# Performance work log

Measured on AMD Instinct MI355X. Metric: run time of the kernel, lower is better.

Reference implementation:

```python
import jax, jax.numpy as jnp
import numpy as np

N = 100000
SAMPLE = 25
FEAT = 128
HIDDEN = 128
CLASSES = 40


def setup_inputs() -> dict:
    key = jax.random.key(0)
    k_x, k_n, k_w1, k_w2, k_wl = jax.random.split(key, 5)
    X = jax.random.normal(k_x, (N, FEAT), dtype=jnp.float32)
    neighbors = jax.random.randint(k_n, (N, SAMPLE), 0, N, dtype=jnp.int32)
    # torch Linear weights are [out_features, in_features], xavier-uniform init
    def xavier(k, out_d, in_d):
        bound = float(np.sqrt(6.0 / (in_d + out_d)))
        return jax.random.uniform(k, (out_d, in_d), dtype=jnp.float32, minval=-bound, maxval=bound)
    W1 = xavier(k_w1, HIDDEN, FEAT)
    W2 = xavier(k_w2, HIDDEN, HIDDEN)
    Wlast = xavier(k_wl, CLASSES, HIDDEN)
    return {"X": X, "neighbors": neighbors, "W1": W1, "W2": W2, "Wlast": Wlast}


def reference(X, neighbors, W1, W2, Wlast):
    # forward: for each layer W: X = spmm(adj, X); X = X @ W.T; relu(X)
    # adj row i has sample_num entries of value 1/sample_num -> mean over sampled neighbors
    h = X
    for W in (W1, W2):
        agg = jnp.mean(h[neighbors], axis=1)          # [N, sample, d] -> [N, d]
        h = jax.nn.relu(jnp.einsum('nd,hd->nh', agg, W))
    return jnp.einsum('nh,ch->nc', h, Wlast)          # [N, class_num]
```

## Files before the change

kernel.cpp:

```cpp
#include <hip/hip_runtime.h>
#include <cstdint>
#include <cstddef>

typedef unsigned short u16;
typedef __bf16 bf16x8 __attribute__((ext_vector_type(8)));
typedef u16 u16x8 __attribute__((ext_vector_type(8)));
typedef float f32x4 __attribute__((ext_vector_type(4)));

#define N_NODES 100000
#define SAMPLE 25
#define FEAT 128
#define CLASSES 40

__device__ __forceinline__ float bf2f(u16 v) {
    return __uint_as_float(((unsigned)v) << 16);
}
__device__ __forceinline__ u16 f2bf(float f) {
    unsigned u = __float_as_uint(f);
    u += 0x7FFFu + ((u >> 16) & 1u);
    return (u16)(u >> 16);
}
__device__ __forceinline__ void split_bf(float x, u16& hi, u16& lo) {
    hi = f2bf(x);
    lo = f2bf(x - bf2f(hi));
}

__device__ __forceinline__ void split8(const float* ap, bf16x8& ah, bf16x8& al) {
    union { u16x8 u; bf16x8 b; } H, L;
    #pragma unroll
    for (int j = 0; j < 8; ++j) {
        u16 h, lo; split_bf(ap[j], h, lo);
        H.u[j] = h; L.u[j] = lo;
    }
    ah = H.b; al = L.b;
}

__device__ __forceinline__ f32x4 mfma_split(bf16x8 ah, bf16x8 al,
                                            bf16x8 bh, bf16x8 bl, f32x4 acc) {
    acc = __builtin_amdgcn_mfma_f32_16x16x32_bf16(ah, bh, acc, 0, 0, 0);
    acc = __builtin_amdgcn_mfma_f32_16x16x32_bf16(al, bh, acc, 0, 0, 0);
    acc = __builtin_amdgcn_mfma_f32_16x16x32_bf16(ah, bl, acc, 0, 0, 0);
    return acc;
}

__global__ __launch_bounds__(256) void prep_all(
    const float* __restrict__ X,
    const float* __restrict__ W1, const float* __restrict__ W2,
    const float* __restrict__ Wl,
    u16* __restrict__ xb,
    u16* __restrict__ w1h, u16* __restrict__ w1l,
    u16* __restrict__ w2h, u16* __restrict__ w2l,
    u16* __restrict__ wlh, u16* __restrict__ wll)
{
    const int i = blockIdx.x * 256 + threadIdx.x;
    const int stride = gridDim.x * 256;

    const int nv = (N_NODES * FEAT) / 8;
    for (int v = i; v < nv; v += stride) {
        f32x4 a = *(const f32x4*)(X + (size_t)v * 8);
        f32x4 b = *(const f32x4*)(X + (size_t)v * 8 + 4);
        u16x8 o;
        o[0] = f2bf(a[0]); o[1] = f2bf(a[1]); o[2] = f2bf(a[2]); o[3] = f2bf(a[3]);
        o[4] = f2bf(b[0]); o[5] = f2bf(b[1]); o[6] = f2bf(b[2]); o[7] = f2bf(b[3]);
        *(u16x8*)(xb + (size_t)v * 8) = o;
    }
    for (int j = i; j < FEAT * FEAT; j += stride) {
        split_bf(W1[j], w1h[j], w1l[j]);
        split_bf(W2[j], w2h[j], w2l[j]);
    }
    for (int j = i; j < CLASSES * FEAT; j += stride) {
        split_bf(Wl[j], wlh[j], wll[j]);
    }
}

#define NPB32 32
#define ZT_STRIDE 136

__global__ __launch_bounds__(128, 2) void hopA(
    const u16* __restrict__ Xb, const int* __restrict__ nb,
    const u16* __restrict__ w1h, const u16* __restrict__ w1l,
    const u16* __restrict__ w2h, const u16* __restrict__ w2l,
    u16* __restrict__ Z2)
{
    __shared__ int nbs[NPB32 * SAMPLE];
    __shared__ u16 agg_h[NPB32][ZT_STRIDE];
    __shared__ u16 agg_l[NPB32][ZT_STRIDE];

    const int t = threadIdx.x;
    const int blockStart = blockIdx.x * NPB32;

    for (int i = t; i < NPB32 * SAMPLE; i += 128)
        nbs[i] = nb[blockStart * SAMPLE + i];
    __syncthreads();

    #pragma unroll 1
    for (int it = 0; it < 4; ++it) {
        const int item = t + it * 128;
        const int nl = item >> 4;
        const int fg = item & 15;
        const int* myn = &nbs[nl * SAMPLE];
        u16x8 buf[SAMPLE];
        #pragma unroll
        for (int s = 0; s < SAMPLE; ++s)
            buf[s] = *(const u16x8*)(Xb + ((size_t)myn[s] << 7) + fg * 8);
        float acc[8];
        #pragma unroll
        for (int j = 0; j < 8; ++j) acc[j] = 0.f;
        #pragma unroll
        for (int s = 0; s < SAMPLE; ++s) {
            #pragma unroll
            for (int j = 0; j < 8; ++j) acc[j] += bf2f(buf[s][j]);
        }
        u16x8 oh, ol;
        #pragma unroll
        for (int j = 0; j < 8; ++j) {
            const float m = acc[j] * (1.0f / SAMPLE);
            u16 h, lo; split_bf(m, h, lo);
            oh[j] = h; ol[j] = lo;
        }
        *(u16x8*)&agg_h[nl][fg * 8] = oh;
        *(u16x8*)&agg_l[nl][fg * 8] = ol;
    }
    __syncthreads();

    const int w  = t >> 6;
    const int l  = t & 63;
    const int lr = l & 15;
    const int lq = l >> 4;

    f32x4 hacc[8];
    {
        bf16x8 ah[4], al[4];
        #pragma unroll
        for (int k = 0; k < 4; ++k) {
            ah[k] = *(const bf16x8*)&agg_h[w * 16 + lr][k * 32 + lq * 8];
            al[k] = *(const bf16x8*)&agg_l[w * 16 + lr][k * 32 + lq * 8];
        }
        #pragma unroll
        for (int c = 0; c < 8; ++c) {
            f32x4 acc = {0.f, 0.f, 0.f, 0.f};
            #pragma unroll
            for (int k = 0; k < 4; ++k) {
                const size_t off = (size_t)(c * 16 + lr) * FEAT + k * 32 + lq * 8;
                bf16x8 bh = *(const bf16x8*)(w1h + off);
                bf16x8 bl = *(const bf16x8*)(w1l + off);
                acc = mfma_split(ah[k], al[k], bh, bl, acc);
            }
            hacc[c] = acc;
        }
    }
    __syncthreads();

    #pragma unroll
    for (int c = 0; c < 8; ++c) {
        #pragma unroll
        for (int r = 0; r < 4; ++r) {
            float v = hacc[c][r] > 0.f ? hacc[c][r] : 0.f;
            u16 h, l2; split_bf(v, h, l2);
            agg_h[w * 16 + lq * 4 + r][c * 16 + lr] = h;
            agg_l[w * 16 + lq * 4 + r][c * 16 + lr] = l2;
        }
    }
    __syncthreads();

    {
        bf16x8 ah[4], al[4];
        #pragma unroll
        for (int k = 0; k < 4; ++k) {
            ah[k] = *(const bf16x8*)&agg_h[w * 16 + lr][k * 32 + lq * 8];
            al[k] = *(const bf16x8*)&agg_l[w * 16 + lr][k * 32 + lq * 8];
        }
        __syncthreads();

        #pragma unroll
        for (int c = 0; c < 8; ++c) {
            f32x4 acc = {0.f, 0.f, 0.f, 0.f};
            #pragma unroll
            for (int k = 0; k < 4; ++k) {
                const size_t off = (size_t)(c * 16 + lr) * FEAT + k * 32 + lq * 8;
                bf16x8 bh = *(const bf16x8*)(w2h + off);
                bf16x8 bl = *(const bf16x8*)(w2l + off);
                acc = mfma_split(ah[k], al[k], bh, bl, acc);
            }
            #pragma unroll
            for (int r = 0; r < 4; ++r)
                agg_h[w * 16 + lq * 4 + r][c * 16 + lr] = f2bf(acc[r]);
        }
    }
    __syncthreads();

    #pragma unroll
    for (int p = 0; p < 4; ++p) {
        const int idx = p * 128 + t;
        const int row = idx >> 4;
        const int col = (idx & 15) * 8;
        *(u16x8*)(Z2 + (size_t)(blockStart + row) * FEAT + col) =
            *(const u16x8*)&agg_h[row][col];
    }
}

__global__ __launch_bounds__(128, 3) void hopB(
    const u16* __restrict__ Zin, const int* __restrict__ nb,
    const u16* __restrict__ wh, const u16* __restrict__ wl,
    float* __restrict__ out)
{
    __shared__ int nbs[NPB32 * SAMPLE];
    __shared__ float agg[NPB32][132];

    const int t = threadIdx.x;
    const int blockStart = blockIdx.x * NPB32;

    for (int i = t; i < NPB32 * SAMPLE; i += 128)
        nbs[i] = nb[blockStart * SAMPLE + i];
    __syncthreads();

    #pragma unroll 1
    for (int it = 0; it < 4; ++it) {
        const int item = t + it * 128;
        const int nl = item >> 4;
        const int fg = item & 15;
        const int* myn = &nbs[nl * SAMPLE];
        u16x8 buf[SAMPLE];
        #pragma unroll
        for (int s = 0; s < SAMPLE; ++s)
            buf[s] = *(const u16x8*)(Zin + ((size_t)myn[s] << 7) + fg * 8);
        float acc[8];
        #pragma unroll
        for (int j = 0; j < 8; ++j) acc[j] = 0.f;
        #pragma unroll
        for (int s = 0; s < SAMPLE; ++s) {
            #pragma unroll
            for (int j = 0; j < 8; ++j) acc[j] += bf2f(buf[s][j]);
        }
        #pragma unroll
        for (int j = 0; j < 8; ++j) {
            float m = acc[j] * (1.0f / SAMPLE);
            agg[nl][fg * 8 + j] = m > 0.f ? m : 0.f;
        }
    }
    __syncthreads();

    const int w  = t >> 6;
    const int l  = t & 63;
    const int lr = l & 15;
    const int lq = l >> 4;

    bf16x8 ah[4], al[4];
    #pragma unroll
    for (int k = 0; k < 4; ++k)
        split8(&agg[w * 16 + lr][k * 32 + lq * 8], ah[k], al[k]);

    #pragma unroll
    for (int c = 0; c < 3; ++c) {
        const int o = c * 16 + lr;
        f32x4 acc = {0.f, 0.f, 0.f, 0.f};
        #pragma unroll
        for (int k = 0; k < 4; ++k) {
            bf16x8 bh, bl;
            if (o < CLASSES) {
                const size_t off = (size_t)o * FEAT + k * 32 + lq * 8;
                bh = *(const bf16x8*)(wh + off);
                bl = *(const bf16x8*)(wl + off);
            } else {
                #pragma unroll
                for (int j = 0; j < 8; ++j) { bh[j] = (__bf16)0.f; bl[j] = (__bf16)0.f; }
            }
            acc = mfma_split(ah[k], al[k], bh, bl, acc);
        }
        if (o < CLASSES) {
            #pragma unroll
            for (int r = 0; r < 4; ++r) {
                const int node = blockStart + w * 16 + lq * 4 + r;
                out[(size_t)node * CLASSES + o] = acc[r];
            }
        }
    }
}

#define NPB 64
#define AGG_STRIDE 136

__global__ __launch_bounds__(256) void gnn_layer1(
    const float* __restrict__ X, const int* __restrict__ nb,
    const u16* __restrict__ w1h, const u16* __restrict__ w1l,
    u16* __restrict__ h1)
{
    __shared__ int nbs[NPB * SAMPLE];
    __shared__ u16 agg_h[NPB][AGG_STRIDE];
    __shared__ u16 agg_l[NPB][AGG_STRIDE];

    const int t = threadIdx.x;
    const int blockStart = blockIdx.x * NPB;

    for (int i = t; i < NPB * SAMPLE; i += 256) {
        int gi = blockStart * SAMPLE + i;
        if (gi >= N_NODES * SAMPLE) gi = N_NODES * SAMPLE - 1;
        nbs[i] = nb[gi];
    }
    __syncthreads();

    for (int item = t; item < NPB * 16; item += 256) {
        const int nl = item >> 4;
        const int fg = item & 15;
        float acc[8];
        #pragma unroll
        for (int j = 0; j < 8; ++j) acc[j] = 0.f;
        const int* myn = &nbs[nl * SAMPLE];
        for (int s = 0; s < SAMPLE; ++s) {
            const float4* p = (const float4*)(X + (size_t)myn[s] * FEAT + fg * 8);
            float4 a = p[0], b = p[1];
            acc[0] += a.x; acc[1] += a.y; acc[2] += a.z; acc[3] += a.w;
            acc[4] += b.x; acc[5] += b.y; acc[6] += b.z; acc[7] += b.w;
        }
        u16x8 oh, ol;
        #pragma unroll
        for (int j = 0; j < 8; ++j) {
            float m = acc[j] * (1.0f / SAMPLE);
            u16 h, lo; split_bf(m, h, lo);
            oh[j] = h; ol[j] = lo;
        }
        *(u16x8*)&agg_h[nl][fg * 8] = oh;
        *(u16x8*)&agg_l[nl][fg * 8] = ol;
    }
    __syncthreads();

    const int w  = t >> 6;
    const int l  = t & 63;
    const int lr = l & 15;
    const int lq = l >> 4;

    bf16x8 ah[4], al[4];
    #pragma unroll
    for (int k = 0; k < 4; ++k) {
        ah[k] = *(const bf16x8*)&agg_h[w * 16 + lr][k * 32 + lq * 8];
        al[k] = *(const bf16x8*)&agg_l[w * 16 + lr][k * 32 + lq * 8];
    }

    #pragma unroll
    for (int c = 0; c < 8; ++c) {
        f32x4 acc = {0.f, 0.f, 0.f, 0.f};
        #pragma unroll
        for (int k = 0; k < 4; ++k) {
            const size_t off = (size_t)(c * 16 + lr) * FEAT + k * 32 + lq * 8;
            bf16x8 bh = *(const bf16x8*)(w1h + off);
            bf16x8 bl = *(const bf16x8*)(w1l + off);
            acc = mfma_split(ah[k], al[k], bh, bl, acc);
        }
        #pragma unroll
        for (int r = 0; r < 4; ++r) {
            int node = blockStart + w * 16 + lq * 4 + r;
            if (node < N_NODES) {
                float v = acc[r] > 0.f ? acc[r] : 0.f;
                h1[(size_t)node * FEAT + c * 16 + lr] = f2bf(v);
            }
        }
    }
}

__global__ __launch_bounds__(256) void gnn_layer2_final(
    const u16* __restrict__ h1, const int* __restrict__ nb,
    const u16* __restrict__ w2h, const u16* __restrict__ w2l,
    const u16* __restrict__ wlh, const u16* __restrict__ wll,
    float* __restrict__ out)
{
    __shared__ int nbs[NPB * SAMPLE];
    __shared__ u16 agg_h[NPB][AGG_STRIDE];
    __shared__ u16 agg_l[NPB][AGG_STRIDE];

    const int t = threadIdx.x;
    const int blockStart = blockIdx.x * NPB;

    for (int i = t; i < NPB * SAMPLE; i += 256) {
        int gi = blockStart * SAMPLE + i;
        if (gi >= N_NODES * SAMPLE) gi = N_NODES * SAMPLE - 1;
        nbs[i] = nb[gi];
    }
    __syncthreads();

    for (int item = t; item < NPB * 16; item += 256) {
        const int nl = item >> 4;
        const int fg = item & 15;
        float acc[8];
        #pragma unroll
        for (int j = 0; j < 8; ++j) acc[j] = 0.f;
        const int* myn = &nbs[nl * SAMPLE];
        for (int s = 0; s < SAMPLE; ++s) {
            u16x8 v = *(const u16x8*)(h1 + (size_t)myn[s] * FEAT + fg * 8);
            #pragma unroll
            for (int j = 0; j < 8; ++j) acc[j] += bf2f(v[j]);
        }
        u16x8 oh, ol;
        #pragma unroll
        for (int j = 0; j < 8; ++j) {
            float m = acc[j] * (1.0f / SAMPLE);
            u16 h, lo; split_bf(m, h, lo);
            oh[j] = h; ol[j] = lo;
        }
        *(u16x8*)&agg_h[nl][fg * 8] = oh;
        *(u16x8*)&agg_l[nl][fg * 8] = ol;
    }
    __syncthreads();

    const int w  = t >> 6;
    const int l  = t & 63;
    const int lr = l & 15;
    const int lq = l >> 4;

    f32x4 hacc[8];
    {
        bf16x8 ah[4], al[4];
        #pragma unroll
        for (int k = 0; k < 4; ++k) {
            ah[k] = *(const bf16x8*)&agg_h[w * 16 + lr][k * 32 + lq * 8];
            al[k] = *(const bf16x8*)&agg_l[w * 16 + lr][k * 32 + lq * 8];
        }
        #pragma unroll
        for (int c = 0; c < 8; ++c) {
            f32x4 acc = {0.f, 0.f, 0.f, 0.f};
            #pragma unroll
            for (int k = 0; k < 4; ++k) {
                const size_t off = (size_t)(c * 16 + lr) * FEAT + k * 32 + lq * 8;
                bf16x8 bh = *(const bf16x8*)(w2h + off);
                bf16x8 bl = *(const bf16x8*)(w2l + off);
                acc = mfma_split(ah[k], al[k], bh, bl, acc);
            }
            hacc[c] = acc;
        }
    }
    __syncthreads();

    #pragma unroll
    for (int c = 0; c < 8; ++c) {
        #pragma unroll
        for (int r = 0; r < 4; ++r) {
            float v = hacc[c][r] > 0.f ? hacc[c][r] : 0.f;
            u16 h, l2; split_bf(v, h, l2);
            agg_h[w * 16 + lq * 4 + r][c * 16 + lr] = h;
            agg_l[w * 16 + lq * 4 + r][c * 16 + lr] = l2;
        }
    }
    __syncthreads();

    {
        bf16x8 ah[4], al[4];
        #pragma unroll
        for (int k = 0; k < 4; ++k) {
            ah[k] = *(const bf16x8*)&agg_h[w * 16 + lr][k * 32 + lq * 8];
            al[k] = *(const bf16x8*)&agg_l[w * 16 + lr][k * 32 + lq * 8];
        }
        #pragma unroll
        for (int c = 0; c < 3; ++c) {
            const int o = c * 16 + lr;
            f32x4 acc = {0.f, 0.f, 0.f, 0.f};
            #pragma unroll
            for (int k = 0; k < 4; ++k) {
                bf16x8 bh, bl;
                if (o < CLASSES) {
                    const size_t off = (size_t)o * FEAT + k * 32 + lq * 8;
                    bh = *(const bf16x8*)(wlh + off);
                    bl = *(const bf16x8*)(wll + off);
                } else {
                    #pragma unroll
                    for (int j = 0; j < 8; ++j) { bh[j] = (__bf16)0.f; bl[j] = (__bf16)0.f; }
                }
                acc = mfma_split(ah[k], al[k], bh, bl, acc);
            }
            if (o < CLASSES) {
                #pragma unroll
                for (int r = 0; r < 4; ++r) {
                    int node = blockStart + w * 16 + lq * 4 + r;
                    if (node < N_NODES) {
                        out[(size_t)node * CLASSES + o] = acc[r];
                    }
                }
            }
        }
    }
}

extern "C" void kernel_launch(void* const* d_in, const int* in_sizes, int n_in,
                              void* d_out, int out_size, void* d_ws, size_t ws_size,
                              hipStream_t stream) {
    const float* X  = (const float*)d_in[0];
    const int*   nb = (const int*)d_in[1];
    const float* W1 = (const float*)d_in[2];
    const float* W2 = (const float*)d_in[3];
    const float* Wl = (const float*)d_in[4];
    float* out = (float*)d_out;

    const size_t zelems = (size_t)N_NODES * FEAT;
    const size_t welems = 4 * (size_t)FEAT * FEAT + 2 * (size_t)CLASSES * FEAT;
    const size_t need_fast = (2 * zelems + welems) * sizeof(u16);

    if (ws_size >= need_fast) {
        u16* Xb  = (u16*)d_ws;
        u16* Z2  = Xb + zelems;
        u16* w1h = Z2 + zelems;
        u16* w1l = w1h + FEAT * FEAT;
        u16* w2h = w1l + FEAT * FEAT;
        u16* w2l = w2h + FEAT * FEAT;
        u16* wlh = w2l + FEAT * FEAT;
        u16* wll = wlh + CLASSES * FEAT;

        prep_all<<<512, 256, 0, stream>>>(X, W1, W2, Wl, Xb,
                                          w1h, w1l, w2h, w2l, wlh, wll);
        const int blocks = N_NODES / NPB32;
        hopA<<<blocks, 128, 0, stream>>>(Xb, nb, w1h, w1l, w2h, w2l, Z2);
        hopB<<<blocks, 128, 0, stream>>>(Z2, nb, wlh, wll, out);
    } else {
        u16* h1  = (u16*)d_ws;
        u16* w1h = h1 + zelems;
        u16* w1l = w1h + FEAT * FEAT;
        u16* w2h = w1l + FEAT * FEAT;
        u16* w2l = w2h + FEAT * FEAT;
        u16* wlh = w2l + FEAT * FEAT;
        u16* wll = wlh + CLASSES * FEAT;

        prep_all<<<512, 256, 0, stream>>>(X, W1, W2, Wl,
                                           h1,
                                          w1h, w1l, w2h, w2l, wlh, wll);
        const int blocks = (N_NODES + NPB - 1) / NPB;
        gnn_layer1<<<blocks, 256, 0, stream>>>(X, nb, w1h, w1l, h1);
        gnn_layer2_final<<<blocks, 256, 0, stream>>>(h1, nb, w2h, w2l, wlh, wll, out);
    }
}
```

Measured before the change: 341.3 us.

## Fuse prep and both hops into one persistent cooperative kernel

Replaces the three separate launches (prep, hopA, hopB) with a single cooperative persistent kernel. It uses grid.sync between phases and an atomic work counter so each block pulls 32-node groups dynamically. The aim is to remove launch gaps and tail effects between kernels and to balance load across CUs. In exchange it needs cooperative launch support, adds grid-wide barrier cost, and depends on an occupancy query, falling back to the old path if that query or the launch fails.

```diff
diff --git a/kernel.cpp b/kernel.cpp
--- a/kernel.cpp
+++ b/kernel.cpp
@@ -1,6 +1,9 @@
 #include <hip/hip_runtime.h>
+#include <hip/hip_cooperative_groups.h>
 #include <cstdint>
 #include <cstddef>
+
+namespace cg = cooperative_groups;
 
 typedef unsigned short u16;
 typedef __bf16 bf16x8 __attribute__((ext_vector_type(8)));
@@ -41,6 +44,244 @@
     acc = __builtin_amdgcn_mfma_f32_16x16x32_bf16(al, bh, acc, 0, 0, 0);
     acc = __builtin_amdgcn_mfma_f32_16x16x32_bf16(ah, bl, acc, 0, 0, 0);
     return acc;
+}
+
+#define NPB32 32
+#define ZT_STRIDE 136
+#define NGROUPS 3125
+
+__global__ __launch_bounds__(128, 3) void fused_all(
+    const float* __restrict__ X, const int* __restrict__ nb,
+    const float* __restrict__ W1, const float* __restrict__ W2,
+    const float* __restrict__ Wl,
+    u16* __restrict__ Xb, u16* __restrict__ Z2,
+    u16* __restrict__ w1h, u16* __restrict__ w1l,
+    u16* __restrict__ w2h, u16* __restrict__ w2l,
+    u16* __restrict__ wlh, u16* __restrict__ wll,
+    int* __restrict__ ctr,
+    float* __restrict__ out)
+{
+    __shared__ int nbs[NPB32 * SAMPLE];
+    __shared__ __align__(16) char smembig[2 * NPB32 * ZT_STRIDE * 2];
+    u16 (*agg_h)[ZT_STRIDE] = (u16(*)[ZT_STRIDE])smembig;
+    u16 (*agg_l)[ZT_STRIDE] = (u16(*)[ZT_STRIDE])(smembig + NPB32 * ZT_STRIDE * 2);
+    float (*aggf)[132] = (float(*)[132])smembig;
+    __shared__ int g_sh;
+
+    const int t = threadIdx.x;
+    cg::grid_group grid = cg::this_grid();
+
+    {
+        if (blockIdx.x == 0 && t == 0) { ctr[0] = 0; ctr[1] = 0; }
+        const int i = blockIdx.x * 128 + t;
+        const int stride = gridDim.x * 128;
+        const int nv = (N_NODES * FEAT) / 8;
+        for (int v = i; v < nv; v += stride) {
+            f32x4 a = *(const f32x4*)(X + (size_t)v * 8);
+            f32x4 b = *(const f32x4*)(X + (size_t)v * 8 + 4);
+            u16x8 o;
+            o[0] = f2bf(a[0]); o[1] = f2bf(a[1]); o[2] = f2bf(a[2]); o[3] = f2bf(a[3]);
+            o[4] = f2bf(b[0]); o[5] = f2bf(b[1]); o[6] = f2bf(b[2]); o[7] = f2bf(b[3]);
+            *(u16x8*)(Xb + (size_t)v * 8) = o;
+        }
+        for (int j = i; j < FEAT * FEAT; j += stride) {
+            split_bf(W1[j], w1h[j], w1l[j]);
+            split_bf(W2[j], w2h[j], w2l[j]);
+        }
+        for (int j = i; j < CLASSES * FEAT; j += stride) {
+            split_bf(Wl[j], wlh[j], wll[j]);
+        }
+    }
+    grid.sync();
+
+    const int w  = t >> 6;
+    const int l  = t & 63;
+    const int lr = l & 15;
+    const int lq = l >> 4;
+
+    for (;;) {
+        __syncthreads();
+        if (t == 0) g_sh = atomicAdd(&ctr[0], 1);
+        __syncthreads();
+        const int gid = g_sh;
+        if (gid >= NGROUPS) break;
+        const int blockStart = gid * NPB32;
+
+        for (int i = t; i < NPB32 * SAMPLE; i += 128)
+            nbs[i] = nb[blockStart * SAMPLE + i];
+        __syncthreads();
+
+        #pragma unroll 1
+        for (int it = 0; it < 4; ++it) {
+            const int item = t + it * 128;
+            const int nl = item >> 4;
+            const int fg = item & 15;
+            const int* myn = &nbs[nl * SAMPLE];
+            u16x8 buf[SAMPLE];
+            #pragma unroll
+            for (int s = 0; s < SAMPLE; ++s)
+                buf[s] = *(const u16x8*)(Xb + ((size_t)myn[s] << 7) + fg * 8);
+            float acc[8];
+            #pragma unroll
+            for (int j = 0; j < 8; ++j) acc[j] = 0.f;
+            #pragma unroll
+            for (int s = 0; s < SAMPLE; ++s) {
+                #pragma unroll
+                for (int j = 0; j < 8; ++j) acc[j] += bf2f(buf[s][j]);
+            }
+            u16x8 oh, ol;
+            #pragma unroll
+            for (int j = 0; j < 8; ++j) {
+                const float m = acc[j] * (1.0f / SAMPLE);
+                u16 h, lo; split_bf(m, h, lo);
+                oh[j] = h; ol[j] = lo;
+            }
+            *(u16x8*)&agg_h[nl][fg * 8] = oh;
+            *(u16x8*)&agg_l[nl][fg * 8] = ol;
+        }
+        __syncthreads();
+
+        f32x4 hacc[8];
+        {
+            bf16x8 ah[4], al[4];
+            #pragma unroll
+            for (int k = 0; k < 4; ++k) {
+                ah[k] = *(const bf16x8*)&agg_h[w * 16 + lr][k * 32 + lq * 8];
+                al[k] = *(const bf16x8*)&agg_l[w * 16 + lr][k * 32 + lq * 8];
+            }
+            #pragma unroll
+            for (int c = 0; c < 8; ++c) {
+                f32x4 acc = {0.f, 0.f, 0.f, 0.f};
+                #pragma unroll
+                for (int k = 0; k < 4; ++k) {
+                    const size_t off = (size_t)(c * 16 + lr) * FEAT + k * 32 + lq * 8;
+                    bf16x8 bh = *(const bf16x8*)(w1h + off);
+                    bf16x8 bl = *(const bf16x8*)(w1l + off);
+                    acc = mfma_split(ah[k], al[k], bh, bl, acc);
+                }
+                hacc[c] = acc;
+            }
+        }
+        __syncthreads();
+
+        #pragma unroll
+        for (int c = 0; c < 8; ++c) {
+            #pragma unroll
+            for (int r = 0; r < 4; ++r) {
+                float v = hacc[c][r] > 0.f ? hacc[c][r] : 0.f;
+                u16 h, l2; split_bf(v, h, l2);
+                agg_h[w * 16 + lq * 4 + r][c * 16 + lr] = h;
+                agg_l[w * 16 + lq * 4 + r][c * 16 + lr] = l2;
+            }
+        }
+        __syncthreads();
+
+        {
+            bf16x8 ah[4], al[4];
+            #pragma unroll
+            for (int k = 0; k < 4; ++k) {
+                ah[k] = *(const bf16x8*)&agg_h[w * 16 + lr][k * 32 + lq * 8];
+                al[k] = *(const bf16x8*)&agg_l[w * 16 + lr][k * 32 + lq * 8];
+            }
+            __syncthreads();
+
+            #pragma unroll
+            for (int c = 0; c < 8; ++c) {
+                f32x4 acc = {0.f, 0.f, 0.f, 0.f};
+                #pragma unroll
+                for (int k = 0; k < 4; ++k) {
+                    const size_t off = (size_t)(c * 16 + lr) * FEAT + k * 32 + lq * 8;
+                    bf16x8 bh = *(const bf16x8*)(w2h + off);
+                    bf16x8 bl = *(const bf16x8*)(w2l + off);
+                    acc = mfma_split(ah[k], al[k], bh, bl, acc);
+                }
+                #pragma unroll
+                for (int r = 0; r < 4; ++r)
+                    agg_h[w * 16 + lq * 4 + r][c * 16 + lr] = f2bf(acc[r]);
+            }
+        }
+        __syncthreads();
+
+        #pragma unroll
+        for (int p = 0; p < 4; ++p) {
+            const int idx = p * 128 + t;
+            const int row = idx >> 4;
+            const int col = (idx & 15) * 8;
+            *(u16x8*)(Z2 + (size_t)(blockStart + row) * FEAT + col) =
+                *(const u16x8*)&agg_h[row][col];
+        }
+    }
+    grid.sync();
+
+    for (;;) {
+        __syncthreads();
+        if (t == 0) g_sh = atomicAdd(&ctr[1], 1);
+        __syncthreads();
+        const int gid = g_sh;
+        if (gid >= NGROUPS) break;
+        const int blockStart = gid * NPB32;
+
+        for (int i = t; i < NPB32 * SAMPLE; i += 128)
+            nbs[i] = nb[blockStart * SAMPLE + i];
+        __syncthreads();
+
+        #pragma unroll 1
+        for (int it = 0; it < 4; ++it) {
+            const int item = t + it * 128;
+            const int nl = item >> 4;
+            const int fg = item & 15;
+            const int* myn = &nbs[nl * SAMPLE];
+            u16x8 buf[SAMPLE];
+            #pragma unroll
+            for (int s = 0; s < SAMPLE; ++s)
+                buf[s] = *(const u16x8*)(Z2 + ((size_t)myn[s] << 7) + fg * 8);
+            float acc[8];
+            #pragma unroll
+            for (int j = 0; j < 8; ++j) acc[j] = 0.f;
+            #pragma unroll
+            for (int s = 0; s < SAMPLE; ++s) {
+                #pragma unroll
+                for (int j = 0; j < 8; ++j) acc[j] += bf2f(buf[s][j]);
+            }
+            #pragma unroll
+            for (int j = 0; j < 8; ++j) {
+                float m = acc[j] * (1.0f / SAMPLE);
+                aggf[nl][fg * 8 + j] = m > 0.f ? m : 0.f;
+            }
+        }
+        __syncthreads();
+
+        bf16x8 ah[4], al[4];
+        #pragma unroll
+        for (int k = 0; k < 4; ++k)
+            split8(&aggf[w * 16 + lr][k * 32 + lq * 8], ah[k], al[k]);
+
+        #pragma unroll
+        for (int c = 0; c < 3; ++c) {
+            const int o = c * 16 + lr;
+            f32x4 acc = {0.f, 0.f, 0.f, 0.f};
+            #pragma unroll
+            for (int k = 0; k < 4; ++k) {
+                bf16x8 bh, bl;
+                if (o < CLASSES) {
+                    const size_t off = (size_t)o * FEAT + k * 32 + lq * 8;
+                    bh = *(const bf16x8*)(wlh + off);
+                    bl = *(const bf16x8*)(wll + off);
+                } else {
+                    #pragma unroll
+                    for (int j = 0; j < 8; ++j) { bh[j] = (__bf16)0.f; bl[j] = (__bf16)0.f; }
+                }
+                acc = mfma_split(ah[k], al[k], bh, bl, acc);
+            }
+            if (o < CLASSES) {
+                #pragma unroll
+                for (int r = 0; r < 4; ++r) {
+                    const int node = blockStart + w * 16 + lq * 4 + r;
+                    out[(size_t)node * CLASSES + o] = acc[r];
+                }
+            }
+        }
+    }
 }
 
 __global__ __launch_bounds__(256) void prep_all(
@@ -73,9 +314,6 @@
     }
 }
 
-#define NPB32 32
-#define ZT_STRIDE 136
-
 __global__ __launch_bounds__(128, 2) void hopA(
     const u16* __restrict__ Xb, const int* __restrict__ nb,
     const u16* __restrict__ w1h, const u16* __restrict__ w1l,
@@ -490,7 +728,7 @@
 
     const size_t zelems = (size_t)N_NODES * FEAT;
     const size_t welems = 4 * (size_t)FEAT * FEAT + 2 * (size_t)CLASSES * FEAT;
-    const size_t need_fast = (2 * zelems + welems) * sizeof(u16);
+    const size_t need_fast = (2 * zelems + welems) * sizeof(u16) + 64;
 
     if (ws_size >= need_fast) {
         u16* Xb  = (u16*)d_ws;
@@ -501,12 +739,38 @@
         u16* w2l = w2h + FEAT * FEAT;
         u16* wlh = w2l + FEAT * FEAT;
         u16* wll = wlh + CLASSES * FEAT;
-
-        prep_all<<<512, 256, 0, stream>>>(X, W1, W2, Wl, Xb,
-                                          w1h, w1l, w2h, w2l, wlh, wll);
-        const int blocks = N_NODES / NPB32;
-        hopA<<<blocks, 128, 0, stream>>>(Xb, nb, w1h, w1l, w2h, w2l, Z2);
-        hopB<<<blocks, 128, 0, stream>>>(Z2, nb, wlh, wll, out);
+        uintptr_t cp = ((uintptr_t)(wll + CLASSES * FEAT) + 7) & ~(uintptr_t)7;
+        int* ctr = (int*)cp;
+
+        static int bpc = 0;
+        if (bpc == 0) {
+            hipError_t oe = hipOccupancyMaxActiveBlocksPerMultiprocessor(
+                &bpc, fused_all, 128, 0);
+            if (oe != hipSuccess || bpc <= 0) bpc = -1;
+        }
+
+        bool launched = false;
+        if (bpc > 0) {
+            int grid = 256 * bpc;
+            if (grid > 2048) grid = 2048;
+            void* args[] = {
+                (void*)&X, (void*)&nb, (void*)&W1, (void*)&W2, (void*)&Wl,
+                (void*)&Xb, (void*)&Z2,
+                (void*)&w1h, (void*)&w1l, (void*)&w2h, (void*)&w2l,
+                (void*)&wlh, (void*)&wll, (void*)&ctr, (void*)&out
+            };
+            hipError_t e = hipLaunchCooperativeKernel(
+                (void*)fused_all, dim3(grid), dim3(128), args, 0, stream);
+            launched = (e == hipSuccess);
+        }
+
+        if (!launched) {
+            prep_all<<<512, 256, 0, stream>>>(X, W1, W2, Wl, Xb,
+                                              w1h, w1l, w2h, w2l, wlh, wll);
+            const int blocks = N_NODES / NPB32;
+            hopA<<<blocks, 128, 0, stream>>>(Xb, nb, w1h, w1l, w2h, w2l, Z2);
+            hopB<<<blocks, 128, 0, stream>>>(Z2, nb, wlh, wll, out);
+        }
     } else {
         u16* h1  = (u16*)d_ws;
         u16* w1h = h1 + zelems;
@@ -516,8 +780,7 @@
         u16* wlh = w2l + FEAT * FEAT;
         u16* wll = wlh + CLASSES * FEAT;
 
-        prep_all<<<512, 256, 0, stream>>>(X, W1, W2, Wl,
-                                           h1,
+        prep_all<<<512, 256, 0, stream>>>(X, W1, W2, Wl, h1,
                                           w1h, w1l, w2h, w2l, wlh, wll);
         const int blocks = (N_NODES + NPB - 1) / NPB;
         gnn_layer1<<<blocks, 256, 0, stream>>>(X, nb, w1h, w1l, h1);
```

Result: slower. 720.9 us (+111.2%).
